# Kernel optimization log

Hardware: AMD Instinct MI355X
Metric: run time of the kernel (lower is better)

The kernel has to match this reference:

```python
import jax, jax.numpy as jnp
import numpy as np

N_NODES = 50000
N_EDGES = 800000
NUM_GRAPHS = 256
F_IN = 64        # num_features (per-head out dim == in dim in this module)
HEADS = 4        # n_heads1
OUT_DIM = 128    # output_dim
HC = HEADS * F_IN
NEG_SLOPE = 0.2  # GATConv leaky_relu slope
EPS = 1e-5       # GraphNorm eps


def setup_inputs() -> dict:
    key = jax.random.key(0)
    ks = jax.random.split(key, 12)
    s = lambda k, shape, fan: (jax.random.normal(k, shape, jnp.float32) / np.sqrt(fan).astype(np.float32))
    return {
        "x": jax.random.normal(ks[0], (N_NODES, F_IN), jnp.float32),
        "edge_index": jax.random.randint(ks[1], (2, N_EDGES), 0, N_NODES),
        "batch": jnp.sort(jax.random.randint(ks[2], (N_NODES,), 0, NUM_GRAPHS)),
        # GATConv params
        "lin_w": s(ks[3], (HC, F_IN), F_IN),
        "att_src": s(ks[4], (HEADS, F_IN), F_IN),
        "att_dst": s(ks[5], (HEADS, F_IN), F_IN),
        "gat_bias": jnp.zeros((HC,), jnp.float32),
        # GraphNorm params
        "gn_weight": jnp.ones((HC,), jnp.float32),
        "gn_bias": jnp.zeros((HC,), jnp.float32),
        "gn_mean_scale": jnp.ones((HC,), jnp.float32),
        # fc_g1 / out heads
        "fc1_w": s(ks[6], (OUT_DIM, HC), HC), "fc1_b": jnp.zeros((OUT_DIM,), jnp.float32),
        "out_w": s(ks[7], (1, OUT_DIM), OUT_DIM), "out_b": jnp.zeros((1,), jnp.float32),
        # GlobalAttention gate_nn: Linear(HC,16) -> ReLU -> Linear(16,1) -> Sigmoid
        "att1_w": s(ks[8], (16, HC), HC), "att1_b": jnp.zeros((16,), jnp.float32),
        "att2_w": s(ks[9], (1, 16), 16), "att2_b": jnp.zeros((1,), jnp.float32),
    }


def _gat_conv(x, edge_index, lin_w, att_src, att_dst, gat_bias):
    """PyG GATConv with add_self_loops=True, concat heads. Returns (out [N,HC], alpha [E+N,H])."""
    N = x.shape[0]
    xh = (x @ lin_w.T).reshape(N, HEADS, F_IN)                 # [N,H,C]
    a_src = (xh * att_src[None]).sum(-1)                        # [N,H]
    a_dst = (xh * att_dst[None]).sum(-1)                        # [N,H]
    loops = jnp.arange(N)
    src = jnp.concatenate([edge_index[0], loops])               # [E+N]
    dst = jnp.concatenate([edge_index[1], loops])
    alpha = jax.nn.leaky_relu(a_src[src] + a_dst[dst], NEG_SLOPE)  # [E+N,H]
    # segment softmax over incoming edges of each dst node (self-loops guarantee non-empty)
    amax = jax.ops.segment_max(alpha, dst, num_segments=N)
    alpha = jnp.exp(alpha - amax[dst])
    denom = jax.ops.segment_sum(alpha, dst, num_segments=N)
    alpha = alpha / (denom[dst] + 1e-16)
    msg = xh[src] * alpha[:, :, None]                           # [E+N,H,C]
    out = jax.ops.segment_sum(msg, dst, num_segments=N).reshape(N, HC) + gat_bias
    return out, alpha


def _graph_norm(x, batch, weight, bias, mean_scale):
    ones = jnp.ones((x.shape[0],), x.dtype)
    cnt = jnp.maximum(jax.ops.segment_sum(ones, batch, num_segments=NUM_GRAPHS), 1.0)[:, None]
    mean = jax.ops.segment_sum(x, batch, num_segments=NUM_GRAPHS) / cnt
    sub = x - mean[batch] * mean_scale
    var = jax.ops.segment_sum(sub * sub, batch, num_segments=NUM_GRAPHS) / cnt
    return weight * sub / jnp.sqrt(var + EPS)[batch] + bias


def _global_attention(x, batch, att1_w, att1_b, att2_w, att2_b):
    gate = jax.nn.sigmoid(jax.nn.relu(x @ att1_w.T + att1_b) @ att2_w.T + att2_b)  # [N,1]
    gmax = jax.ops.segment_max(gate, batch, num_segments=NUM_GRAPHS)
    gate = jnp.exp(gate - gmax[batch])
    gden = jax.ops.segment_sum(gate, batch, num_segments=NUM_GRAPHS)
    gate = gate / (gden[batch] + 1e-16)
    return jax.ops.segment_sum(gate * x, batch, num_segments=NUM_GRAPHS)  # [G,HC]


def reference(x, edge_index, batch, lin_w, att_src, att_dst, gat_bias,
              gn_weight, gn_bias, gn_mean_scale, fc1_w, fc1_b, out_w, out_b,
              att1_w, att1_b, att2_w, att2_b):
    x2, alpha = _gat_conv(x, edge_index, lin_w, att_src, att_dst, gat_bias)
    h = _graph_norm(x2, batch, gn_weight, gn_bias, gn_mean_scale)
    h = jax.nn.relu(h)                                # node_dropout = identity (eval)
    pooled = _global_attention(h, batch, att1_w, att1_b, att2_w, att2_b)
    h = jax.nn.relu(pooled @ fc1_w.T + fc1_b)          # dropout = identity (eval)
    out = jax.nn.sigmoid(h @ out_w.T + out_b)          # [G,1]
    return out, alpha
```

## Files before the change

### kernel.cpp

```cpp
#include <hip/hip_runtime.h>
#include <hip/hip_fp16.h>
#include <math.h>

#define NN 50000
#define NE 800000
#define NG 256
#define NEG_SLOPE 0.2f
#define GEPS 1e-5f
#define CHUNK 64
#define NB 196
#define CAP 6144
#define EPB 3125
#define SPLIT 8

typedef _Float16 f16x8 __attribute__((ext_vector_type(8)));
typedef _Float16 f16x4 __attribute__((ext_vector_type(4)));
typedef float f32x4 __attribute__((ext_vector_type(4)));
typedef float f32x2 __attribute__((ext_vector_type(2)));

__device__ __forceinline__ float lrelu(float v){ return v > 0.f ? v : NEG_SLOPE * v; }

__global__ __launch_bounds__(256) void k_misc(const float* __restrict__ lin_w,
                                              _Float16* __restrict__ wh,
                                              const float* __restrict__ att1_w,
                                              _Float16* __restrict__ a1w,
                                              const int* __restrict__ batch,
                                              int* __restrict__ goff,
                                              int* __restrict__ gcnt,
                                              int* __restrict__ bucket_cnt) {
  int b = blockIdx.x, tid = threadIdx.x;
  if (b == 0) {
    if (tid < NB) bucket_cnt[tid] = 0;
    int g = tid;
    int lo = 0, hi = NN;
    while (lo < hi) { int mid = (lo + hi) >> 1; if (batch[mid] < g) lo = mid + 1; else hi = mid; }
    int start = lo;
    lo = 0; hi = NN;
    while (lo < hi) { int mid = (lo + hi) >> 1; if (batch[mid] < g + 1) lo = mid + 1; else hi = mid; }
    goff[g] = start;
    gcnt[g] = lo - start;
  } else if (b <= 16) {
    int i0 = (b - 1) * 1024 + tid * 4;
    float4 f = *(const float4*)&lin_w[i0];
    f16x4 h4;
    h4[0] = (_Float16)f.x; h4[1] = (_Float16)f.y; h4[2] = (_Float16)f.z; h4[3] = (_Float16)f.w;
    *(f16x4*)&wh[i0] = h4;
  } else {
    int i0 = (b - 17) * 1024 + tid * 4;
    float4 f = *(const float4*)&att1_w[i0];
    f16x4 h4;
    h4[0] = (_Float16)f.x; h4[1] = (_Float16)f.y; h4[2] = (_Float16)f.z; h4[3] = (_Float16)f.w;
    *(f16x4*)&a1w[i0] = h4;
  }
}

__global__ __launch_bounds__(256) void k_lin(const float* __restrict__ x,
                                             const _Float16* __restrict__ wh,
                                             const float* __restrict__ att_src,
                                             const float* __restrict__ att_dst,
                                             unsigned char* __restrict__ xh8,
                                             float* __restrict__ a_src_n,
                                             float* __restrict__ a_dst_n) {
  __shared__ unsigned char s_f8[4 * 4096];
  int w = threadIdx.x >> 6, lane = threadIdx.x & 63;
  int nb = blockIdx.x * 64 + w * 16;
  if (nb >= NN) return;
  int am = lane & 15, quad = lane >> 4;
  int wb = w * 4096;

  const float* xr = x + (size_t)(nb + am) * 64 + quad * 8;
  float4 f0 = *(const float4*)(xr);
  float4 f1 = *(const float4*)(xr + 4);
  float4 f2 = *(const float4*)(xr + 32);
  float4 f3 = *(const float4*)(xr + 36);
  f16x8 a0, a1;
  a0[0] = (_Float16)f0.x; a0[1] = (_Float16)f0.y; a0[2] = (_Float16)f0.z; a0[3] = (_Float16)f0.w;
  a0[4] = (_Float16)f1.x; a0[5] = (_Float16)f1.y; a0[6] = (_Float16)f1.z; a0[7] = (_Float16)f1.w;
  a1[0] = (_Float16)f2.x; a1[1] = (_Float16)f2.y; a1[2] = (_Float16)f2.z; a1[3] = (_Float16)f2.w;
  a1[4] = (_Float16)f3.x; a1[5] = (_Float16)f3.y; a1[6] = (_Float16)f3.z; a1[7] = (_Float16)f3.w;

  f32x4 acc[16];
#pragma unroll
  for (int ct = 0; ct < 16; ct++) acc[ct] = (f32x4){0.f, 0.f, 0.f, 0.f};

#pragma unroll
  for (int ct = 0; ct < 16; ct++) {
    const _Float16* wbp = wh + (size_t)(ct * 16 + am) * 64 + quad * 8;
    f16x8 b0 = *(const f16x8*)(wbp);
    f16x8 b1 = *(const f16x8*)(wbp + 32);
    acc[ct] = __builtin_amdgcn_mfma_f32_16x16x32_f16(a0, b0, acc[ct], 0, 0, 0);
    acc[ct] = __builtin_amdgcn_mfma_f32_16x16x32_f16(a1, b1, acc[ct], 0, 0, 0);
  }

  float ps[4][4], pd[4][4];
#pragma unroll
  for (int r = 0; r < 4; r++)
#pragma unroll
    for (int h = 0; h < 4; h++) { ps[r][h] = 0.f; pd[r][h] = 0.f; }
#pragma unroll
  for (int ct = 0; ct < 16; ct++) {
    int c = ct * 16 + am;
    float av = att_src[c];
    float dv = att_dst[c];
    int h = ct >> 2;
#pragma unroll
    for (int r = 0; r < 4; r++) {
      float v = acc[ct][r];
      ps[r][h] += v * av;
      pd[r][h] += v * dv;
    }
  }
#pragma unroll
  for (int r = 0; r < 4; r++)
#pragma unroll
    for (int h = 0; h < 4; h++) {
      float s = ps[r][h], d = pd[r][h];
#pragma unroll
      for (int o = 1; o < 16; o <<= 1) {
        s += __shfl_xor(s, o, 64);
        d += __shfl_xor(d, o, 64);
      }
      if (am == 0) {
        int node = nb + quad * 4 + r;
        a_src_n[node * 4 + h] = s;
        a_dst_n[node * 4 + h] = d;
      }
    }

#pragma unroll
  for (int r = 0; r < 4; r++) {
    uint4 u;
    int t;
    t = __builtin_amdgcn_cvt_pk_fp8_f32(acc[0][r],  acc[1][r],  0, 0);
    t = __builtin_amdgcn_cvt_pk_fp8_f32(acc[2][r],  acc[3][r],  t, 1);
    u.x = (unsigned)t;
    t = __builtin_amdgcn_cvt_pk_fp8_f32(acc[4][r],  acc[5][r],  0, 0);
    t = __builtin_amdgcn_cvt_pk_fp8_f32(acc[6][r],  acc[7][r],  t, 1);
    u.y = (unsigned)t;
    t = __builtin_amdgcn_cvt_pk_fp8_f32(acc[8][r],  acc[9][r],  0, 0);
    t = __builtin_amdgcn_cvt_pk_fp8_f32(acc[10][r], acc[11][r], t, 1);
    u.z = (unsigned)t;
    t = __builtin_amdgcn_cvt_pk_fp8_f32(acc[12][r], acc[13][r], 0, 0);
    t = __builtin_amdgcn_cvt_pk_fp8_f32(acc[14][r], acc[15][r], t, 1);
    u.w = (unsigned)t;
    *(uint4*)&s_f8[wb + (quad * 4 + r) * 256 + am * 16] = u;
  }
#pragma unroll
  for (int p = 0; p < 4; p++) {
    uint4 u = *(const uint4*)&s_f8[wb + p * 1024 + lane * 16];
    *(uint4*)&xh8[(size_t)nb * 256 + p * 1024 + lane * 16] = u;
  }
}

__global__ __launch_bounds__(256) void k_binA(const int* __restrict__ ei,
                                              int* __restrict__ bucket_cnt,
                                              int2* __restrict__ ebuf) {
  __shared__ int2 sorted[EPB];
  __shared__ int hist[NB];
  __shared__ int lbase[NB];
  __shared__ int cur[NB];
  __shared__ int runb[NB];
  __shared__ int wsum[4];
  int b = blockIdx.x, tid = threadIdx.x, lane = tid & 63, wid = tid >> 6;
  int e0 = b * EPB, e1 = min(e0 + EPB, NE);
  int n = e1 - e0;
  for (int i = tid; i < NB; i += 256) hist[i] = 0;
  __syncthreads();
  for (int e = e0 + tid; e < e1; e += 256) atomicAdd(&hist[ei[NE + e] >> 8], 1);
  __syncthreads();
  {
    int v = (tid < NB) ? hist[tid] : 0;
    int s = v;
#pragma unroll
    for (int o = 1; o < 64; o <<= 1) { int t = __shfl_up(s, o, 64); if (lane >= o) s += t; }
    if (lane == 63) wsum[wid] = s;
    __syncthreads();
    int wbase = 0;
    for (int k = 0; k < wid; k++) wbase += wsum[k];
    if (tid < NB) {
      int ex = wbase + s - v;
      lbase[tid] = ex;
      cur[tid] = ex;
      runb[tid] = atomicAdd(&bucket_cnt[tid], v);
    }
  }
  __syncthreads();
  for (int e = e0 + tid; e < e1; e += 256) {
    int d = ei[NE + e], s = ei[e];
    int lp = atomicAdd(&cur[d >> 8], 1);
    sorted[lp] = make_int2(d, s);
  }
  __syncthreads();
  for (int i = tid; i < n; i += 256) {
    int2 e = sorted[i];
    int bk = e.x >> 8;
    int slot = runb[bk] + (i - lbase[bk]);
    if (slot < CAP) ebuf[(size_t)bk * CAP + slot] = e;
  }
}

__global__ __launch_bounds__(256) void k_bscan(const int* __restrict__ bucket_cnt,
                                               int* __restrict__ bucket_base) {
  __shared__ int wsum[4];
  int tid = threadIdx.x, lane = tid & 63, wid = tid >> 6;
  int v = (tid < NB) ? min(bucket_cnt[tid], CAP) : 0;
  int s = v;
#pragma unroll
  for (int o = 1; o < 64; o <<= 1) { int t = __shfl_up(s, o, 64); if (lane >= o) s += t; }
  if (lane == 63) wsum[wid] = s;
  __syncthreads();
  int wbase = 0;
  for (int k = 0; k < wid; k++) wbase += wsum[k];
  if (tid < NB) bucket_base[tid] = wbase + s - v;
}

__global__ __launch_bounds__(256) void k_binB(const int2* __restrict__ ebuf,
                                              const int* __restrict__ bucket_cnt,
                                              const int* __restrict__ bucket_base,
                                              int* __restrict__ deg,
                                              int* __restrict__ offs,
                                              int* __restrict__ src_list) {
  __shared__ int hist[256];
  __shared__ int cur[256];
  __shared__ int wsum[4];
  int b = blockIdx.x, tid = threadIdx.x, lane = tid & 63, wid = tid >> 6;
  int cnt = min(bucket_cnt[b], CAP);
  int base = bucket_base[b];
  const int2* seg = ebuf + (size_t)b * CAP;
  hist[tid] = 0;
  __syncthreads();
  for (int i = tid; i < cnt; i += 256) atomicAdd(&hist[seg[i].x & 255], 1);
  __syncthreads();
  int v = hist[tid];
  int s = v;
#pragma unroll
  for (int o = 1; o < 64; o <<= 1) { int t = __shfl_up(s, o, 64); if (lane >= o) s += t; }
  if (lane == 63) wsum[wid] = s;
  __syncthreads();
  int wbase = 0;
  for (int k = 0; k < wid; k++) wbase += wsum[k];
  int excl = wbase + s - v;
  int node = b * 256 + tid;
  if (node < NN) {
    deg[node] = v;
    offs[node] = base + excl;
  }
  cur[tid] = excl;
  __syncthreads();
  for (int i = tid; i < cnt; i += 256) {
    int2 e = seg[i];
    int pos = base + atomicAdd(&cur[e.x & 255], 1);
    src_list[pos] = e.y;
  }
}

__global__ __launch_bounds__(64) void k_gat(const unsigned char* __restrict__ xh8,
                                            const float* __restrict__ a_src_n,
                                            const float* __restrict__ a_dst_n,
                                            const int* __restrict__ offs,
                                            const int* __restrict__ deg_arr,
                                            const int* __restrict__ src_list,
                                            const float* __restrict__ gat_bias,
                                            __half* __restrict__ x2h,
                                            float* __restrict__ den_inv) {
  __shared__ __align__(16) float s_al[CHUNK * 4];
  __shared__ int s_src[CHUNK];
  __shared__ __half s_tr[256];
  int n = blockIdx.x, lane = threadIdx.x;
  int off = offs[n], dg = deg_arr[n], cnt = dg + 1;
  float4 ad = *(const float4*)&a_dst_n[n * 4];
  int h = lane & 3;
  float acc0 = 0.f, acc1 = 0.f, acc2 = 0.f, acc3 = 0.f;

  if (cnt <= 64) {
    float e0 = 0.f, e1 = 0.f, e2 = 0.f, e3 = 0.f;
    if (lane < cnt) {
      int src = (lane < dg) ? src_list[off + lane] : n;
      float4 as = *(const float4*)&a_src_n[src * 4];
      e0 = __expf(lrelu(as.x + ad.x));
      e1 = __expf(lrelu(as.y + ad.y));
      e2 = __expf(lrelu(as.z + ad.z));
      e3 = __expf(lrelu(as.w + ad.w));
      s_src[lane] = src;
    }
    float s0 = e0, s1 = e1, s2 = e2, s3 = e3;
#pragma unroll
    for (int o = 32; o >= 1; o >>= 1) {
      s0 += __shfl_xor(s0, o, 64);
      s1 += __shfl_xor(s1, o, 64);
      s2 += __shfl_xor(s2, o, 64);
      s3 += __shfl_xor(s3, o, 64);
    }
    float i0 = 1.f / (s0 + 1e-16f), i1 = 1.f / (s1 + 1e-16f);
    float i2 = 1.f / (s2 + 1e-16f), i3 = 1.f / (s3 + 1e-16f);
    if (lane == 0) *(float4*)&den_inv[n * 4] = make_float4(i0, i1, i2, i3);
    if (lane < cnt) {
      s_al[lane * 4 + 0] = e0 * i0;
      s_al[lane * 4 + 1] = e1 * i1;
      s_al[lane * 4 + 2] = e2 * i2;
      s_al[lane * 4 + 3] = e3 * i3;
    }
    __syncthreads();
    int j = 0;
    for (; j + 4 <= cnt; j += 4) {
      int sA = s_src[j], sB = s_src[j + 1], sC = s_src[j + 2], sD = s_src[j + 3];
      unsigned rA = *(const unsigned*)&xh8[(size_t)sA * 256 + 4 * lane];
      unsigned rB = *(const unsigned*)&xh8[(size_t)sB * 256 + 4 * lane];
      unsigned rC = *(const unsigned*)&xh8[(size_t)sC * 256 + 4 * lane];
      unsigned rD = *(const unsigned*)&xh8[(size_t)sD * 256 + 4 * lane];
      float aA = s_al[j * 4 + h], aB = s_al[(j + 1) * 4 + h];
      float aC = s_al[(j + 2) * 4 + h], aD = s_al[(j + 3) * 4 + h];
      f32x2 lA = __builtin_amdgcn_cvt_pk_f32_fp8((int)rA, 0);
      f32x2 hA = __builtin_amdgcn_cvt_pk_f32_fp8((int)rA, 1);
      f32x2 lB = __builtin_amdgcn_cvt_pk_f32_fp8((int)rB, 0);
      f32x2 hB = __builtin_amdgcn_cvt_pk_f32_fp8((int)rB, 1);
      f32x2 lC = __builtin_amdgcn_cvt_pk_f32_fp8((int)rC, 0);
      f32x2 hC = __builtin_amdgcn_cvt_pk_f32_fp8((int)rC, 1);
      f32x2 lD = __builtin_amdgcn_cvt_pk_f32_fp8((int)rD, 0);
      f32x2 hD = __builtin_amdgcn_cvt_pk_f32_fp8((int)rD, 1);
      acc0 += aA * lA[0] + aB * lB[0] + aC * lC[0] + aD * lD[0];
      acc1 += aA * lA[1] + aB * lB[1] + aC * lC[1] + aD * lD[1];
      acc2 += aA * hA[0] + aB * hB[0] + aC * hC[0] + aD * hD[0];
      acc3 += aA * hA[1] + aB * hB[1] + aC * hC[1] + aD * hD[1];
    }
    for (; j < cnt; j++) {
      int sA = s_src[j];
      unsigned rA = *(const unsigned*)&xh8[(size_t)sA * 256 + 4 * lane];
      float aA = s_al[j * 4 + h];
      f32x2 lA = __builtin_amdgcn_cvt_pk_f32_fp8((int)rA, 0);
      f32x2 hA = __builtin_amdgcn_cvt_pk_f32_fp8((int)rA, 1);
      acc0 += aA * lA[0];
      acc1 += aA * lA[1];
      acc2 += aA * hA[0];
      acc3 += aA * hA[1];
    }
  } else {
    float s0 = 0.f, s1 = 0.f, s2 = 0.f, s3 = 0.f;
    for (int j = lane; j < cnt; j += 64) {
      int src = (j < dg) ? src_list[off + j] : n;
      float4 as = *(const float4*)&a_src_n[src * 4];
      s0 += __expf(lrelu(as.x + ad.x));
      s1 += __expf(lrelu(as.y + ad.y));
      s2 += __expf(lrelu(as.z + ad.z));
      s3 += __expf(lrelu(as.w + ad.w));
    }
#pragma unroll
    for (int o = 32; o >= 1; o >>= 1) {
      s0 += __shfl_xor(s0, o, 64);
      s1 += __shfl_xor(s1, o, 64);
      s2 += __shfl_xor(s2, o, 64);
      s3 += __shfl_xor(s3, o, 64);
    }
    float i0 = 1.f / (s0 + 1e-16f), i1 = 1.f / (s1 + 1e-16f);
    float i2 = 1.f / (s2 + 1e-16f), i3 = 1.f / (s3 + 1e-16f);
    if (lane == 0) *(float4*)&den_inv[n * 4] = make_float4(i0, i1, i2, i3);
    for (int cb = 0; cb < cnt; cb += CHUNK) {
      int clen = min(CHUNK, cnt - cb);
      for (int j = lane; j < clen; j += 64) {
        int jj = cb + j;
        int src = (jj < dg) ? src_list[off + jj] : n;
        float4 as = *(const float4*)&a_src_n[src * 4];
        s_src[j] = src;
        s_al[j * 4 + 0] = __expf(lrelu(as.x + ad.x)) * i0;
        s_al[j * 4 + 1] = __expf(lrelu(as.y + ad.y)) * i1;
        s_al[j * 4 + 2] = __expf(lrelu(as.z + ad.z)) * i2;
        s_al[j * 4 + 3] = __expf(lrelu(as.w + ad.w)) * i3;
      }
      __syncthreads();
      for (int j = 0; j < clen; j++) {
        int sA = s_src[j];
        unsigned rA = *(const unsigned*)&xh8[(size_t)sA * 256 + 4 * lane];
        float aA = s_al[j * 4 + h];
        f32x2 lA = __builtin_amdgcn_cvt_pk_f32_fp8((int)rA, 0);
        f32x2 hA = __builtin_amdgcn_cvt_pk_f32_fp8((int)rA, 1);
        acc0 += aA * lA[0];
        acc1 += aA * lA[1];
        acc2 += aA * hA[0];
        acc3 += aA * hA[1];
      }
      __syncthreads();
    }
  }

  int cb0 = (lane & 3) * 64 + (lane >> 2);
  s_tr[cb0 +  0] = __float2half(acc0 + gat_bias[cb0 +  0]);
  s_tr[cb0 + 16] = __float2half(acc1 + gat_bias[cb0 + 16]);
  s_tr[cb0 + 32] = __float2half(acc2 + gat_bias[cb0 + 32]);
  s_tr[cb0 + 48] = __float2half(acc3 + gat_bias[cb0 + 48]);
  __syncthreads();
  uint2 u = *(const uint2*)&s_tr[4 * lane];
  *(uint2*)&x2h[(size_t)n * 256 + 4 * lane] = u;
}

__global__ __launch_bounds__(256) void k_alpha(const int* __restrict__ ei,
                                               const float* __restrict__ a_src_n,
                                               const float* __restrict__ a_dst_n,
                                               const float* __restrict__ den_inv,
                                               float* __restrict__ alpha_out) {
  int idx = blockIdx.x * 256 + threadIdx.x;
  if (idx >= NE + NN) return;
  int s, d;
  if (idx < NE) { s = ei[idx]; d = ei[NE + idx]; }
  else          { s = idx - NE; d = s; }
  float4 as = *(const float4*)&a_src_n[s * 4];
  float4 ad = *(const float4*)&a_dst_n[d * 4];
  float4 iv = *(const float4*)&den_inv[d * 4];
  float4 a;
  a.x = __expf(lrelu(as.x + ad.x)) * iv.x;
  a.y = __expf(lrelu(as.y + ad.y)) * iv.y;
  a.z = __expf(lrelu(as.z + ad.z)) * iv.z;
  a.w = __expf(lrelu(as.w + ad.w)) * iv.w;
  *(float4*)&alpha_out[(size_t)idx * 4] = a;
}

__global__ __launch_bounds__(256) void k_stats1(const __half* __restrict__ x2h,
                                                const int* __restrict__ gcnt,
                                                const int* __restrict__ goff,
                                                float* __restrict__ psumA,
                                                float* __restrict__ psumB) {
  int b = blockIdx.x, c = threadIdx.x;
  int g = b >> 3, s = b & 7;
  int cnt = gcnt[g], start = goff[g];
  const __half* p = x2h + (size_t)start * 256 + c;
  float sum = 0.f, sum2 = 0.f;
  int i = s;
  for (; i + 56 < cnt; i += 64) {
    float v0 = __half2float(p[(size_t)(i +  0) * 256]);
    float v1 = __half2float(p[(size_t)(i +  8) * 256]);
    float v2 = __half2float(p[(size_t)(i + 16) * 256]);
    float v3 = __half2float(p[(size_t)(i + 24) * 256]);
    float v4 = __half2float(p[(size_t)(i + 32) * 256]);
    float v5 = __half2float(p[(size_t)(i + 40) * 256]);
    float v6 = __half2float(p[(size_t)(i + 48) * 256]);
    float v7 = __half2float(p[(size_t)(i + 56) * 256]);
    sum += ((v0 + v1) + (v2 + v3)) + ((v4 + v5) + (v6 + v7));
    sum2 += ((v0 * v0 + v1 * v1) + (v2 * v2 + v3 * v3)) +
            ((v4 * v4 + v5 * v5) + (v6 * v6 + v7 * v7));
  }
  for (; i < cnt; i += 8) { float v = __half2float(p[(size_t)i * 256]); sum += v; sum2 += v * v; }
  psumA[b * 256 + c] = sum;
  psumB[b * 256 + c] = sum2;
}

__global__ __launch_bounds__(256) void k_stats2(const float* __restrict__ psumA,
                                                const float* __restrict__ psumB,
                                                const int* __restrict__ gcnt,
                                                const float* __restrict__ gn_w,
                                                const float* __restrict__ gn_b,
                                                const float* __restrict__ gn_ms,
                                                float* __restrict__ scale_g,
                                                float* __restrict__ shift_g) {
  int g = blockIdx.x, c = threadIdx.x;
  int b0 = g * SPLIT;
  float S = 0.f, S2 = 0.f;
#pragma unroll
  for (int k = 0; k < SPLIT; k++) {
    S  += psumA[(b0 + k) * 256 + c];
    S2 += psumB[(b0 + k) * 256 + c];
  }
  float fc = fmaxf((float)gcnt[g], 1.f);
  float mean = S / fc;
  float mm = mean * gn_ms[c];
  float var = fmaxf(S2 / fc - 2.f * mm * mean + mm * mm, 0.f);
  float sc = gn_w[c] / sqrtf(var + GEPS);
  scale_g[g * 256 + c] = sc;
  shift_g[g * 256 + c] = gn_b[c] - sc * mm;
}

__global__ __launch_bounds__(256) void k_gate(const __half* __restrict__ x2h,
                                              const int* __restrict__ batch,
                                              const float* __restrict__ scale_g,
                                              const float* __restrict__ shift_g,
                                              const _Float16* __restrict__ a1w,
                                              const float* __restrict__ att1_b,
                                              const float* __restrict__ att2_w,
                                              const float* __restrict__ att2_b,
                                              float* __restrict__ gate_raw) {
  int w = threadIdx.x >> 6, lane = threadIdx.x & 63;
  int nb = blockIdx.x * 64 + w * 16;
  if (nb >= NN) return;
  int am = lane & 15, quad = lane >> 4;
  int node = nb + am;
  int g = batch[node];

  const __half*   xp  = x2h + (size_t)node * 256 + quad * 8;
  const float*    scp = scale_g + g * 256 + quad * 8;
  const float*    shp = shift_g + g * 256 + quad * 8;
  const _Float16* bp  = a1w + am * 256 + quad * 8;

  f32x4 acc = (f32x4){0.f, 0.f, 0.f, 0.f};
#pragma unroll
  for (int kb = 0; kb < 8; kb++) {
    f16x8 xv = *(const f16x8*)(xp + kb * 32);
    float4 sc0 = *(const float4*)(scp + kb * 32);
    float4 sc1 = *(const float4*)(scp + kb * 32 + 4);
    float4 sh0 = *(const float4*)(shp + kb * 32);
    float4 sh1 = *(const float4*)(shp + kb * 32 + 4);
    f16x8 a;
    a[0] = (_Float16)fmaxf(sc0.x * (float)xv[0] + sh0.x, 0.f);
    a[1] = (_Float16)fmaxf(sc0.y * (float)xv[1] + sh0.y, 0.f);
    a[2] = (_Float16)fmaxf(sc0.z * (float)xv[2] + sh0.z, 0.f);
    a[3] = (_Float16)fmaxf(sc0.w * (float)xv[3] + sh0.w, 0.f);
    a[4] = (_Float16)fmaxf(sc1.x * (float)xv[4] + sh1.x, 0.f);
    a[5] = (_Float16)fmaxf(sc1.y * (float)xv[5] + sh1.y, 0.f);
    a[6] = (_Float16)fmaxf(sc1.z * (float)xv[6] + sh1.z, 0.f);
    a[7] = (_Float16)fmaxf(sc1.w * (float)xv[7] + sh1.w, 0.f);
    f16x8 b = *(const f16x8*)(bp + kb * 32);
    acc = __builtin_amdgcn_mfma_f32_16x16x32_f16(a, b, acc, 0, 0, 0);
  }

  float b1 = att1_b[am], w2 = att2_w[am], b2 = att2_b[0];
#pragma unroll
  for (int r = 0; r < 4; r++) {
    float t = w2 * fmaxf(acc[r] + b1, 0.f);
#pragma unroll
    for (int o = 1; o < 16; o <<= 1) t += __shfl_xor(t, o, 64);
    if (am == 0) gate_raw[nb + quad * 4 + r] = 1.f / (1.f + __expf(-(t + b2)));
  }
}

__global__ __launch_bounds__(256) void k_gsm(const float* __restrict__ gate_raw,
                                             const int* __restrict__ gcnt,
                                             const int* __restrict__ goff,
                                             float* __restrict__ wnorm) {
  __shared__ float red[4];
  int g = blockIdx.x, tid = threadIdx.x, lane = tid & 63, wid = tid >> 6;
  int cnt = gcnt[g], start = goff[g];
  float ls = 0.f;
  for (int i = tid; i < cnt; i += 256) ls += __expf(gate_raw[start + i]);
#pragma unroll
  for (int o = 32; o >= 1; o >>= 1) ls += __shfl_xor(ls, o, 64);
  if (lane == 0) red[wid] = ls;
  __syncthreads();
  float rden = 1.f / (red[0] + red[1] + red[2] + red[3] + 1e-16f);
  for (int i = tid; i < cnt; i += 256) wnorm[start + i] = __expf(gate_raw[start + i]) * rden;
}

__global__ __launch_bounds__(256) void k_poolp(const __half* __restrict__ x2h,
                                               const float* __restrict__ wnorm,
                                               const int* __restrict__ gcnt,
                                               const int* __restrict__ goff,
                                               const float* __restrict__ scale_g,
                                               const float* __restrict__ shift_g,
                                               float* __restrict__ ppool) {
  int b = blockIdx.x, c = threadIdx.x;
  int g = b >> 3, s = b & 7;
  int cnt = gcnt[g], start = goff[g];
  float sc = scale_g[g * 256 + c], sh = shift_g[g * 256 + c];
  const __half* p = x2h + (size_t)start * 256 + c;
  const float* wv = wnorm + start;
  float pooled = 0.f;
  int i = s;
  for (; i + 56 < cnt; i += 64) {
    float v0 = __half2float(p[(size_t)(i +  0) * 256]);
    float v1 = __half2float(p[(size_t)(i +  8) * 256]);
    float v2 = __half2float(p[(size_t)(i + 16) * 256]);
    float v3 = __half2float(p[(size_t)(i + 24) * 256]);
    float v4 = __half2float(p[(size_t)(i + 32) * 256]);
    float v5 = __half2float(p[(size_t)(i + 40) * 256]);
    float v6 = __half2float(p[(size_t)(i + 48) * 256]);
    float v7 = __half2float(p[(size_t)(i + 56) * 256]);
    pooled += wv[i +  0] * fmaxf(sc * v0 + sh, 0.f);
    pooled += wv[i +  8] * fmaxf(sc * v1 + sh, 0.f);
    pooled += wv[i + 16] * fmaxf(sc * v2 + sh, 0.f);
    pooled += wv[i + 24] * fmaxf(sc * v3 + sh, 0.f);
    pooled += wv[i + 32] * fmaxf(sc * v4 + sh, 0.f);
    pooled += wv[i + 40] * fmaxf(sc * v5 + sh, 0.f);
    pooled += wv[i + 48] * fmaxf(sc * v6 + sh, 0.f);
    pooled += wv[i + 56] * fmaxf(sc * v7 + sh, 0.f);
  }
  for (; i < cnt; i += 8)
    pooled += wv[i] * fmaxf(sc * __half2float(p[(size_t)i * 256]) + sh, 0.f);
  ppool[b * 256 + c] = pooled;
}

__global__ __launch_bounds__(256) void k_fin(const float* __restrict__ ppool,
                                             const float* __restrict__ fc1_w,
                                             const float* __restrict__ fc1_b,
                                             const float* __restrict__ out_w,
                                             const float* __restrict__ out_b,
                                             float* __restrict__ outp) {
  __shared__ __align__(16) float pool_s[256];
  __shared__ float hred[128];
  __shared__ float red[4];
  int g = blockIdx.x, tid = threadIdx.x, lane = tid & 63, wid = tid >> 6;
  int b0 = g * SPLIT;
  float acc = 0.f;
#pragma unroll
  for (int k = 0; k < SPLIT; k++) acc += ppool[(b0 + k) * 256 + tid];
  pool_s[tid] = acc;
  __syncthreads();
  float4 psv = *(const float4*)&pool_s[4 * lane];
  for (int j0 = 0; j0 < 32; j0++) {
    int j = wid * 32 + j0;
    float4 w = *(const float4*)&fc1_w[j * 256 + 4 * lane];
    float d = w.x * psv.x + w.y * psv.y + w.z * psv.z + w.w * psv.w;
#pragma unroll
    for (int o = 32; o >= 1; o >>= 1) d += __shfl_xor(d, o, 64);
    if (lane == 0) hred[j] = fmaxf(d + fc1_b[j], 0.f) * out_w[j];
  }
  __syncthreads();
  if (tid < 128) {
    float v = hred[tid];
#pragma unroll
    for (int o = 32; o >= 1; o >>= 1) v += __shfl_xor(v, o, 64);
    if (lane == 0) red[wid] = v;
  }
  __syncthreads();
  if (tid == 0) outp[g] = 1.f / (1.f + __expf(-(red[0] + red[1] + out_b[0])));
}

extern "C" void kernel_launch(void* const* d_in, const int* in_sizes, int n_in,
                              void* d_out, int out_size, void* d_ws, size_t ws_size,
                              hipStream_t stream) {
  const float* x        = (const float*)d_in[0];
  const int*   ei       = (const int*)d_in[1];
  const int*   batch    = (const int*)d_in[2];
  const float* lin_w    = (const float*)d_in[3];
  const float* att_src  = (const float*)d_in[4];
  const float* att_dst  = (const float*)d_in[5];
  const float* gat_bias = (const float*)d_in[6];
  const float* gn_w     = (const float*)d_in[7];
  const float* gn_b     = (const float*)d_in[8];
  const float* gn_ms    = (const float*)d_in[9];
  const float* fc1_w    = (const float*)d_in[10];
  const float* fc1_b    = (const float*)d_in[11];
  const float* out_w    = (const float*)d_in[12];
  const float* out_b    = (const float*)d_in[13];
  const float* att1_w   = (const float*)d_in[14];
  const float* att1_b   = (const float*)d_in[15];
  const float* att2_w   = (const float*)d_in[16];
  const float* att2_b   = (const float*)d_in[17];

  float* outp  = (float*)d_out;
  float* alpha = outp + NG;

  char* wsb = (char*)d_ws;
  size_t o = 0;
  auto A = [&](size_t bytes) -> char* {
    char* p = wsb + o;
    o += (bytes + 255) & ~(size_t)255;
    return p;
  };
  unsigned char* xh8 = (unsigned char*)A((size_t)NN * 256);
  __half*   x2h      = (__half*)A((size_t)NN * 256 * 2);
  _Float16* wh       = (_Float16*)A((size_t)256 * 64 * 2);
  _Float16* a1w      = (_Float16*)A((size_t)16 * 256 * 2);
  float* a_src_n  = (float*)A((size_t)NN * 4 * 4);
  float* a_dst_n  = (float*)A((size_t)NN * 4 * 4);
  float* den_inv  = (float*)A((size_t)NN * 4 * 4);
  float* gate_raw = (float*)A((size_t)NN * 4);
  float* wnorm    = (float*)A((size_t)NN * 4);
  float* psumA    = (float*)A((size_t)NG * SPLIT * 256 * 4);
  float* psumB    = (float*)A((size_t)NG * SPLIT * 256 * 4);
  float* ppool    = (float*)A((size_t)NG * SPLIT * 256 * 4);
  float* scale_g  = (float*)A((size_t)NG * 256 * 4);
  float* shift_g  = (float*)A((size_t)NG * 256 * 4);
  int*   deg      = (int*)A((size_t)NN * 4);
  int*   gcnt     = (int*)A((size_t)NG * 4);
  int*   offs     = (int*)A((size_t)NN * 4);
  int*   goff     = (int*)A((size_t)NG * 4);
  int*   src_list = (int*)A((size_t)NE * 4);
  int2*  ebuf     = (int2*)A((size_t)NB * CAP * 8);
  int*   bucket_cnt  = (int*)A((size_t)NB * 4);
  int*   bucket_base = (int*)A((size_t)NB * 4);

  k_misc<<<21, 256, 0, stream>>>(lin_w, wh, att1_w, a1w, batch, goff, gcnt, bucket_cnt);
  k_lin<<<(NN + 63) / 64, 256, 0, stream>>>(x, wh, att_src, att_dst, xh8, a_src_n, a_dst_n);
  k_binA<<<256, 256, 0, stream>>>(ei, bucket_cnt, ebuf);
  k_bscan<<<1, 256, 0, stream>>>(bucket_cnt, bucket_base);
  k_binB<<<NB, 256, 0, stream>>>(ebuf, bucket_cnt, bucket_base, deg, offs, src_list);
  k_gat<<<NN, 64, 0, stream>>>(xh8, a_src_n, a_dst_n, offs, deg, src_list,
                               gat_bias, x2h, den_inv);
  k_alpha<<<(NE + NN + 255) / 256, 256, 0, stream>>>(ei, a_src_n, a_dst_n, den_inv, alpha);
  k_stats1<<<NG * SPLIT, 256, 0, stream>>>(x2h, gcnt, goff, psumA, psumB);
  k_stats2<<<NG, 256, 0, stream>>>(psumA, psumB, gcnt, gn_w, gn_b, gn_ms, scale_g, shift_g);
  k_gate<<<(NN + 63) / 64, 256, 0, stream>>>(x2h, batch, scale_g, shift_g, a1w, att1_b,
                                             att2_w, att2_b, gate_raw);
  k_gsm<<<NG, 256, 0, stream>>>(gate_raw, gcnt, goff, wnorm);
  k_poolp<<<NG * SPLIT, 256, 0, stream>>>(x2h, wnorm, gcnt, goff, scale_g, shift_g, ppool);
  k_fin<<<NG, 256, 0, stream>>>(ppool, fc1_w, fc1_b, out_w, out_b, outp);
}
```

Before: 264.6 us.

## Merge independent kernels into shared launches and fold gate softmax into pooling

Fuses the linear projection with edge binning phase A into one launch that dispatches on block index, and fuses the alpha writeout with the GraphNorm partial-statistics pass. The bucket prefix scan moves into every binB block, and the gate softmax kernel is removed: each pooling block recomputes the exp weights into shared memory and applies the normalizer at the end. The GAT gather switches to 32-bit offset arithmetic. This cuts four launches and the wnorm buffer round trip. In exchange, work is duplicated across blocks, shared-memory weights are limited to 1024 nodes per graph, and the fused kernels use more shared memory per block.

```diff
diff --git a/kernel.cpp b/kernel.cpp
--- a/kernel.cpp
+++ b/kernel.cpp
@@ -12,6 +12,8 @@
 #define CAP 6144
 #define EPB 3125
 #define SPLIT 8
+#define NLINB 782
+#define ABLK 3321
 
 typedef _Float16 f16x8 __attribute__((ext_vector_type(8)));
 typedef _Float16 f16x4 __attribute__((ext_vector_type(4)));
@@ -54,14 +56,15 @@
   }
 }
 
-__global__ __launch_bounds__(256) void k_lin(const float* __restrict__ x,
-                                             const _Float16* __restrict__ wh,
-                                             const float* __restrict__ att_src,
-                                             const float* __restrict__ att_dst,
-                                             unsigned char* __restrict__ xh8,
-                                             float* __restrict__ a_src_n,
-                                             float* __restrict__ a_dst_n) {
-  __shared__ unsigned char s_f8[4 * 4096];
+__device__ __forceinline__ void lin_body(char* smem,
+                                         const float* __restrict__ x,
+                                         const _Float16* __restrict__ wh,
+                                         const float* __restrict__ att_src,
+                                         const float* __restrict__ att_dst,
+                                         unsigned char* __restrict__ xh8,
+                                         float* __restrict__ a_src_n,
+                                         float* __restrict__ a_dst_n) {
+  unsigned char* s_f8 = (unsigned char*)smem;
   int w = threadIdx.x >> 6, lane = threadIdx.x & 63;
   int nb = blockIdx.x * 64 + w * 16;
   if (nb >= NN) return;
@@ -152,16 +155,17 @@
   }
 }
 
-__global__ __launch_bounds__(256) void k_binA(const int* __restrict__ ei,
-                                              int* __restrict__ bucket_cnt,
-                                              int2* __restrict__ ebuf) {
-  __shared__ int2 sorted[EPB];
-  __shared__ int hist[NB];
-  __shared__ int lbase[NB];
-  __shared__ int cur[NB];
-  __shared__ int runb[NB];
-  __shared__ int wsum[4];
-  int b = blockIdx.x, tid = threadIdx.x, lane = tid & 63, wid = tid >> 6;
+__device__ __forceinline__ void binA_body(char* smem, int b,
+                                          const int* __restrict__ ei,
+                                          int* __restrict__ bucket_cnt,
+                                          int2* __restrict__ ebuf) {
+  int2* sorted = (int2*)smem;
+  int*  hist   = (int*)(smem + 25024);
+  int*  lbase  = (int*)(smem + 25824);
+  int*  cur    = (int*)(smem + 26624);
+  int*  runb   = (int*)(smem + 27424);
+  int*  wsum   = (int*)(smem + 28224);
+  int tid = threadIdx.x, lane = tid & 63, wid = tid >> 6;
   int e0 = b * EPB, e1 = min(e0 + EPB, NE);
   int n = e1 - e0;
   for (int i = tid; i < NB; i += 256) hist[i] = 0;
@@ -199,33 +203,47 @@
   }
 }
 
-__global__ __launch_bounds__(256) void k_bscan(const int* __restrict__ bucket_cnt,
-                                               int* __restrict__ bucket_base) {
-  __shared__ int wsum[4];
-  int tid = threadIdx.x, lane = tid & 63, wid = tid >> 6;
-  int v = (tid < NB) ? min(bucket_cnt[tid], CAP) : 0;
-  int s = v;
-#pragma unroll
-  for (int o = 1; o < 64; o <<= 1) { int t = __shfl_up(s, o, 64); if (lane >= o) s += t; }
-  if (lane == 63) wsum[wid] = s;
-  __syncthreads();
-  int wbase = 0;
-  for (int k = 0; k < wid; k++) wbase += wsum[k];
-  if (tid < NB) bucket_base[tid] = wbase + s - v;
+__global__ __launch_bounds__(256) void k_linbin(const float* __restrict__ x,
+                                                const _Float16* __restrict__ wh,
+                                                const float* __restrict__ att_src,
+                                                const float* __restrict__ att_dst,
+                                                unsigned char* __restrict__ xh8,
+                                                float* __restrict__ a_src_n,
+                                                float* __restrict__ a_dst_n,
+                                                const int* __restrict__ ei,
+                                                int* __restrict__ bucket_cnt,
+                                                int2* __restrict__ ebuf) {
+  __shared__ __align__(16) char smem[28240];
+  if (blockIdx.x < NLINB)
+    lin_body(smem, x, wh, att_src, att_dst, xh8, a_src_n, a_dst_n);
+  else
+    binA_body(smem, blockIdx.x - NLINB, ei, bucket_cnt, ebuf);
 }
 
 __global__ __launch_bounds__(256) void k_binB(const int2* __restrict__ ebuf,
                                               const int* __restrict__ bucket_cnt,
-                                              const int* __restrict__ bucket_base,
                                               int* __restrict__ deg,
                                               int* __restrict__ offs,
                                               int* __restrict__ src_list) {
   __shared__ int hist[256];
   __shared__ int cur[256];
   __shared__ int wsum[4];
+  __shared__ int bbase[NB];
   int b = blockIdx.x, tid = threadIdx.x, lane = tid & 63, wid = tid >> 6;
+  {
+    int v = (tid < NB) ? min(bucket_cnt[tid], CAP) : 0;
+    int s = v;
+#pragma unroll
+    for (int o = 1; o < 64; o <<= 1) { int t = __shfl_up(s, o, 64); if (lane >= o) s += t; }
+    if (lane == 63) wsum[wid] = s;
+    __syncthreads();
+    int wbase = 0;
+    for (int k = 0; k < wid; k++) wbase += wsum[k];
+    if (tid < NB) bbase[tid] = wbase + s - v;
+  }
+  __syncthreads();
   int cnt = min(bucket_cnt[b], CAP);
-  int base = bucket_base[b];
+  int base = bbase[b];
   const int2* seg = ebuf + (size_t)b * CAP;
   hist[tid] = 0;
   __syncthreads();
@@ -270,6 +288,7 @@
   int off = offs[n], dg = deg_arr[n], cnt = dg + 1;
   float4 ad = *(const float4*)&a_dst_n[n * 4];
   int h = lane & 3;
+  unsigned loff = 4u * (unsigned)lane;
   float acc0 = 0.f, acc1 = 0.f, acc2 = 0.f, acc3 = 0.f;
 
   if (cnt <= 64) {
@@ -303,11 +322,14 @@
     __syncthreads();
     int j = 0;
     for (; j + 4 <= cnt; j += 4) {
-      int sA = s_src[j], sB = s_src[j + 1], sC = s_src[j + 2], sD = s_src[j + 3];
-      unsigned rA = *(const unsigned*)&xh8[(size_t)sA * 256 + 4 * lane];
-      unsigned rB = *(const unsigned*)&xh8[(size_t)sB * 256 + 4 * lane];
-      unsigned rC = *(const unsigned*)&xh8[(size_t)sC * 256 + 4 * lane];
-      unsigned rD = *(const unsigned*)&xh8[(size_t)sD * 256 + 4 * lane];
+      unsigned oA = ((unsigned)s_src[j] << 8) + loff;
+      unsigned oB = ((unsigned)s_src[j + 1] << 8) + loff;
+      unsigned oC = ((unsigned)s_src[j + 2] << 8) + loff;
+      unsigned oD = ((unsigned)s_src[j + 3] << 8) + loff;
+      unsigned rA = *(const unsigned*)&xh8[oA];
+      unsigned rB = *(const unsigned*)&xh8[oB];
+      unsigned rC = *(const unsigned*)&xh8[oC];
+      unsigned rD = *(const unsigned*)&xh8[oD];
       float aA = s_al[j * 4 + h], aB = s_al[(j + 1) * 4 + h];
       float aC = s_al[(j + 2) * 4 + h], aD = s_al[(j + 3) * 4 + h];
       f32x2 lA = __builtin_amdgcn_cvt_pk_f32_fp8((int)rA, 0);
@@ -324,8 +346,8 @@
       acc3 += aA * hA[1] + aB * hB[1] + aC * hC[1] + aD * hD[1];
     }
     for (; j < cnt; j++) {
-      int sA = s_src[j];
-      unsigned rA = *(const unsigned*)&xh8[(size_t)sA * 256 + 4 * lane];
+      unsigned oA = ((unsigned)s_src[j] << 8) + loff;
+      unsigned rA = *(const unsigned*)&xh8[oA];
       float aA = s_al[j * 4 + h];
       f32x2 lA = __builtin_amdgcn_cvt_pk_f32_fp8((int)rA, 0);
       f32x2 hA = __builtin_amdgcn_cvt_pk_f32_fp8((int)rA, 1);
@@ -368,8 +390,8 @@
       }
       __syncthreads();
       for (int j = 0; j < clen; j++) {
-        int sA = s_src[j];
-        unsigned rA = *(const unsigned*)&xh8[(size_t)sA * 256 + 4 * lane];
+        unsigned oA = ((unsigned)s_src[j] << 8) + loff;
+        unsigned rA = *(const unsigned*)&xh8[oA];
         float aA = s_al[j * 4 + h];
         f32x2 lA = __builtin_amdgcn_cvt_pk_f32_fp8((int)rA, 0);
         f32x2 hA = __builtin_amdgcn_cvt_pk_f32_fp8((int)rA, 1);
@@ -392,54 +414,55 @@
   *(uint2*)&x2h[(size_t)n * 256 + 4 * lane] = u;
 }
 
-__global__ __launch_bounds__(256) void k_alpha(const int* __restrict__ ei,
-                                               const float* __restrict__ a_src_n,
-                                               const float* __restrict__ a_dst_n,
-                                               const float* __restrict__ den_inv,
-                                               float* __restrict__ alpha_out) {
-  int idx = blockIdx.x * 256 + threadIdx.x;
-  if (idx >= NE + NN) return;
-  int s, d;
-  if (idx < NE) { s = ei[idx]; d = ei[NE + idx]; }
-  else          { s = idx - NE; d = s; }
-  float4 as = *(const float4*)&a_src_n[s * 4];
-  float4 ad = *(const float4*)&a_dst_n[d * 4];
-  float4 iv = *(const float4*)&den_inv[d * 4];
-  float4 a;
-  a.x = __expf(lrelu(as.x + ad.x)) * iv.x;
-  a.y = __expf(lrelu(as.y + ad.y)) * iv.y;
-  a.z = __expf(lrelu(as.z + ad.z)) * iv.z;
-  a.w = __expf(lrelu(as.w + ad.w)) * iv.w;
-  *(float4*)&alpha_out[(size_t)idx * 4] = a;
-}
-
-__global__ __launch_bounds__(256) void k_stats1(const __half* __restrict__ x2h,
-                                                const int* __restrict__ gcnt,
-                                                const int* __restrict__ goff,
-                                                float* __restrict__ psumA,
-                                                float* __restrict__ psumB) {
-  int b = blockIdx.x, c = threadIdx.x;
-  int g = b >> 3, s = b & 7;
-  int cnt = gcnt[g], start = goff[g];
-  const __half* p = x2h + (size_t)start * 256 + c;
-  float sum = 0.f, sum2 = 0.f;
-  int i = s;
-  for (; i + 56 < cnt; i += 64) {
-    float v0 = __half2float(p[(size_t)(i +  0) * 256]);
-    float v1 = __half2float(p[(size_t)(i +  8) * 256]);
-    float v2 = __half2float(p[(size_t)(i + 16) * 256]);
-    float v3 = __half2float(p[(size_t)(i + 24) * 256]);
-    float v4 = __half2float(p[(size_t)(i + 32) * 256]);
-    float v5 = __half2float(p[(size_t)(i + 40) * 256]);
-    float v6 = __half2float(p[(size_t)(i + 48) * 256]);
-    float v7 = __half2float(p[(size_t)(i + 56) * 256]);
-    sum += ((v0 + v1) + (v2 + v3)) + ((v4 + v5) + (v6 + v7));
-    sum2 += ((v0 * v0 + v1 * v1) + (v2 * v2 + v3 * v3)) +
-            ((v4 * v4 + v5 * v5) + (v6 * v6 + v7 * v7));
-  }
-  for (; i < cnt; i += 8) { float v = __half2float(p[(size_t)i * 256]); sum += v; sum2 += v * v; }
-  psumA[b * 256 + c] = sum;
-  psumB[b * 256 + c] = sum2;
+__global__ __launch_bounds__(256) void k_alst(const int* __restrict__ ei,
+                                              const float* __restrict__ a_src_n,
+                                              const float* __restrict__ a_dst_n,
+                                              const float* __restrict__ den_inv,
+                                              float* __restrict__ alpha_out,
+                                              const __half* __restrict__ x2h,
+                                              const int* __restrict__ gcnt,
+                                              const int* __restrict__ goff,
+                                              float* __restrict__ psumA,
+                                              float* __restrict__ psumB) {
+  if (blockIdx.x < ABLK) {
+    int idx = blockIdx.x * 256 + threadIdx.x;
+    if (idx >= NE + NN) return;
+    int s, d;
+    if (idx < NE) { s = ei[idx]; d = ei[NE + idx]; }
+    else          { s = idx - NE; d = s; }
+    float4 as = *(const float4*)&a_src_n[s * 4];
+    float4 ad = *(const float4*)&a_dst_n[d * 4];
+    float4 iv = *(const float4*)&den_inv[d * 4];
+    float4 a;
+    a.x = __expf(lrelu(as.x + ad.x)) * iv.x;
+    a.y = __expf(lrelu(as.y + ad.y)) * iv.y;
+    a.z = __expf(lrelu(as.z + ad.z)) * iv.z;
+    a.w = __expf(lrelu(as.w + ad.w)) * iv.w;
+    *(float4*)&alpha_out[(size_t)idx * 4] = a;
+  } else {
+    int b = blockIdx.x - ABLK, c = threadIdx.x;
+    int g = b >> 3, s = b & 7;
+    int cnt = gcnt[g], start = goff[g];
+    const __half* p = x2h + (size_t)start * 256 + c;
+    float sum = 0.f, sum2 = 0.f;
+    int i = s;
+    for (; i + 56 < cnt; i += 64) {
+      float v0 = __half2float(p[(size_t)(i +  0) * 256]);
+      float v1 = __half2float(p[(size_t)(i +  8) * 256]);
+      float v2 = __half2float(p[(size_t)(i + 16) * 256]);
+      float v3 = __half2float(p[(size_t)(i + 24) * 256]);
+      float v4 = __half2float(p[(size_t)(i + 32) * 256]);
+      float v5 = __half2float(p[(size_t)(i + 40) * 256]);
+      float v6 = __half2float(p[(size_t)(i + 48) * 256]);
+      float v7 = __half2float(p[(size_t)(i + 56) * 256]);
+      sum += ((v0 + v1) + (v2 + v3)) + ((v4 + v5) + (v6 + v7));
+      sum2 += ((v0 * v0 + v1 * v1) + (v2 * v2 + v3 * v3)) +
+              ((v4 * v4 + v5 * v5) + (v6 * v6 + v7 * v7));
+    }
+    for (; i < cnt; i += 8) { float v = __half2float(p[(size_t)i * 256]); sum += v; sum2 += v * v; }
+    psumA[b * 256 + c] = sum;
+    psumB[b * 256 + c] = sum2;
+  }
 }
 
 __global__ __launch_bounds__(256) void k_stats2(const float* __restrict__ psumA,
@@ -519,36 +542,32 @@
   }
 }
 
-__global__ __launch_bounds__(256) void k_gsm(const float* __restrict__ gate_raw,
-                                             const int* __restrict__ gcnt,
-                                             const int* __restrict__ goff,
-                                             float* __restrict__ wnorm) {
-  __shared__ float red[4];
-  int g = blockIdx.x, tid = threadIdx.x, lane = tid & 63, wid = tid >> 6;
-  int cnt = gcnt[g], start = goff[g];
-  float ls = 0.f;
-  for (int i = tid; i < cnt; i += 256) ls += __expf(gate_raw[start + i]);
-#pragma unroll
-  for (int o = 32; o >= 1; o >>= 1) ls += __shfl_xor(ls, o, 64);
-  if (lane == 0) red[wid] = ls;
-  __syncthreads();
-  float rden = 1.f / (red[0] + red[1] + red[2] + red[3] + 1e-16f);
-  for (int i = tid; i < cnt; i += 256) wnorm[start + i] = __expf(gate_raw[start + i]) * rden;
-}
-
 __global__ __launch_bounds__(256) void k_poolp(const __half* __restrict__ x2h,
-                                               const float* __restrict__ wnorm,
+                                               const float* __restrict__ gate_raw,
                                                const int* __restrict__ gcnt,
                                                const int* __restrict__ goff,
                                                const float* __restrict__ scale_g,
                                                const float* __restrict__ shift_g,
                                                float* __restrict__ ppool) {
-  int b = blockIdx.x, c = threadIdx.x;
+  __shared__ float s_w[1024];
+  __shared__ float red[4];
+  int b = blockIdx.x, c = threadIdx.x, lane = c & 63, wid = c >> 6;
   int g = b >> 3, s = b & 7;
   int cnt = gcnt[g], start = goff[g];
+  float ls = 0.f;
+  for (int i = c; i < cnt; i += 256) {
+    float e = __expf(gate_raw[start + i]);
+    s_w[i] = e;
+    ls += e;
+  }
+#pragma unroll
+  for (int o = 32; o >= 1; o >>= 1) ls += __shfl_xor(ls, o, 64);
+  if (lane == 0) red[wid] = ls;
+  __syncthreads();
+  float rden = 1.f / (red[0] + red[1] + red[2] + red[3] + 1e-16f);
+
   float sc = scale_g[g * 256 + c], sh = shift_g[g * 256 + c];
   const __half* p = x2h + (size_t)start * 256 + c;
-  const float* wv = wnorm + start;
   float pooled = 0.f;
   int i = s;
   for (; i + 56 < cnt; i += 64) {
@@ -560,18 +579,18 @@
     float v5 = __half2float(p[(size_t)(i + 40) * 256]);
     float v6 = __half2float(p[(size_t)(i + 48) * 256]);
     float v7 = __half2float(p[(size_t)(i + 56) * 256]);
-    pooled += wv[i +  0] * fmaxf(sc * v0 + sh, 0.f);
-    pooled += wv[i +  8] * fmaxf(sc * v1 + sh, 0.f);
-    pooled += wv[i + 16] * fmaxf(sc * v2 + sh, 0.f);
-    pooled += wv[i + 24] * fmaxf(sc * v3 + sh, 0.f);
-    pooled += wv[i + 32] * fmaxf(sc * v4 + sh, 0.f);
-    pooled += wv[i + 40] * fmaxf(sc * v5 + sh, 0.f);
-    pooled += wv[i + 48] * fmaxf(sc * v6 + sh, 0.f);
-    pooled += wv[i + 56] * fmaxf(sc * v7 + sh, 0.f);
+    pooled += s_w[i +  0] * fmaxf(sc * v0 + sh, 0.f);
+    pooled += s_w[i +  8] * fmaxf(sc * v1 + sh, 0.f);
+    pooled += s_w[i + 16] * fmaxf(sc * v2 + sh, 0.f);
+    pooled += s_w[i + 24] * fmaxf(sc * v3 + sh, 0.f);
+    pooled += s_w[i + 32] * fmaxf(sc * v4 + sh, 0.f);
+    pooled += s_w[i + 40] * fmaxf(sc * v5 + sh, 0.f);
+    pooled += s_w[i + 48] * fmaxf(sc * v6 + sh, 0.f);
+    pooled += s_w[i + 56] * fmaxf(sc * v7 + sh, 0.f);
   }
   for (; i < cnt; i += 8)
-    pooled += wv[i] * fmaxf(sc * __half2float(p[(size_t)i * 256]) + sh, 0.f);
-  ppool[b * 256 + c] = pooled;
+    pooled += s_w[i] * fmaxf(sc * __half2float(p[(size_t)i * 256]) + sh, 0.f);
+  ppool[b * 256 + c] = pooled * rden;
 }
 
 __global__ __launch_bounds__(256) void k_fin(const float* __restrict__ ppool,
@@ -650,7 +669,6 @@
   float* a_dst_n  = (float*)A((size_t)NN * 4 * 4);
   float* den_inv  = (float*)A((size_t)NN * 4 * 4);
   float* gate_raw = (float*)A((size_t)NN * 4);
-  float* wnorm    = (float*)A((size_t)NN * 4);
   float* psumA    = (float*)A((size_t)NG * SPLIT * 256 * 4);
   float* psumB    = (float*)A((size_t)NG * SPLIT * 256 * 4);
   float* ppool    = (float*)A((size_t)NG * SPLIT * 256 * 4);
@@ -663,21 +681,18 @@
   int*   src_list = (int*)A((size_t)NE * 4);
   int2*  ebuf     = (int2*)A((size_t)NB * CAP * 8);
   int*   bucket_cnt  = (int*)A((size_t)NB * 4);
-  int*   bucket_base = (int*)A((size_t)NB * 4);
 
   k_misc<<<21, 256, 0, stream>>>(lin_w, wh, att1_w, a1w, batch, goff, gcnt, bucket_cnt);
-  k_lin<<<(NN + 63) / 64, 256, 0, stream>>>(x, wh, att_src, att_dst, xh8, a_src_n, a_dst_n);
-  k_binA<<<256, 256, 0, stream>>>(ei, bucket_cnt, ebuf);
-  k_bscan<<<1, 256, 0, stream>>>(bucket_cnt, bucket_base);
-  k_binB<<<NB, 256, 0, stream>>>(ebuf, bucket_cnt, bucket_base, deg, offs, src_list);
+  k_linbin<<<NLINB + 256, 256, 0, stream>>>(x, wh, att_src, att_dst, xh8, a_src_n, a_dst_n,
+                                            ei, bucket_cnt, ebuf);
+  k_binB<<<NB, 256, 0, stream>>>(ebuf, bucket_cnt, deg, offs, src_list);
   k_gat<<<NN, 64, 0, stream>>>(xh8, a_src_n, a_dst_n, offs, deg, src_list,
                                gat_bias, x2h, den_inv);
-  k_alpha<<<(NE + NN + 255) / 256, 256, 0, stream>>>(ei, a_src_n, a_dst_n, den_inv, alpha);
-  k_stats1<<<NG * SPLIT, 256, 0, stream>>>(x2h, gcnt, goff, psumA, psumB);
+  k_alst<<<ABLK + NG * SPLIT, 256, 0, stream>>>(ei, a_src_n, a_dst_n, den_inv, alpha,
+                                                x2h, gcnt, goff, psumA, psumB);
   k_stats2<<<NG, 256, 0, stream>>>(psumA, psumB, gcnt, gn_w, gn_b, gn_ms, scale_g, shift_g);
   k_gate<<<(NN + 63) / 64, 256, 0, stream>>>(x2h, batch, scale_g, shift_g, a1w, att1_b,
                                              att2_w, att2_b, gate_raw);
-  k_gsm<<<NG, 256, 0, stream>>>(gate_raw, gcnt, goff, wnorm);
-  k_poolp<<<NG * SPLIT, 256, 0, stream>>>(x2h, wnorm, gcnt, goff, scale_g, shift_g, ppool);
+  k_poolp<<<NG * SPLIT, 256, 0, stream>>>(x2h, gate_raw, gcnt, goff, scale_g, shift_g, ppool);
   k_fin<<<NG, 256, 0, stream>>>(ppool, fc1_w, fc1_b, out_w, out_b, outp);
 }
```

New measurement: 248.4 us. -6.1%, faster.
